# Kernel tuning notes

Hardware: AMD Instinct MI355X
Metric: run time of the kernel (lower is better)

Reference implementation:

```python
import jax, jax.numpy as jnp
import numpy as np

B, N, C = 4, 2048, 1024
H = 16
HD = C // H
SCALE = HD ** -0.5


def setup_inputs() -> dict:
    key = jax.random.key(0)
    ks = jax.random.split(key, 5)
    s = 0.02
    return {
        "x": jax.random.normal(ks[0], (B, N, C), dtype=jnp.float32),
        "w_qkv": jax.random.normal(ks[1], (C, 3 * C), dtype=jnp.float32) * s,
        "b_qkv": jnp.zeros((3 * C,), dtype=jnp.float32),
        "w_proj": jax.random.normal(ks[2], (C, C), dtype=jnp.float32) * s,
        "b_proj": jnp.zeros((C,), dtype=jnp.float32),
    }


def reference(x, w_qkv, b_qkv, w_proj, b_proj):
    b, n, c = x.shape
    qkv = x @ w_qkv + b_qkv                       # [b, n, 3c]
    qkv = qkv.reshape(b, n, 3, H, HD)
    qkv = jnp.transpose(qkv, (2, 0, 3, 1, 4))     # [3, b, h, n, hd]
    q, k, v = qkv[0], qkv[1], qkv[2]
    attn = jnp.einsum("bhqd,bhkd->bhqk", q, k) * SCALE
    attn = jax.nn.softmax(attn, axis=-1)
    out = jnp.einsum("bhqk,bhkd->bhqd", attn, v)  # [b, h, n, hd]
    out = jnp.transpose(out, (0, 2, 1, 3)).reshape(b, n, c)
    return out @ w_proj + b_proj
```

## Files before the change

### kernel.cpp

```cpp
#include <hip/hip_runtime.h>
#include <cstdint>
#include <cstddef>


typedef __attribute__((ext_vector_type(8))) short short8;
typedef __attribute__((ext_vector_type(4))) float f32x4;
typedef _Float16 half4 __attribute__((ext_vector_type(4)));

#if __has_builtin(__builtin_amdgcn_exp2f)
#define EXP2F(x) __builtin_amdgcn_exp2f(x)
#else
#define EXP2F(x) __expf((x) * 0.69314718056f)
#endif

__device__ __forceinline__ short f2bf(float x) {
  unsigned u = __builtin_bit_cast(unsigned, x);
  u += 0x7fffu + ((u >> 16) & 1u);
  return (short)(u >> 16);
}

__device__ __forceinline__ unsigned pkh(float a, float b) {
  auto h = __builtin_amdgcn_cvt_pkrtz(a, b);
  return __builtin_bit_cast(unsigned, h);
}

__device__ __forceinline__ void async16(const void* g, void* l) {
  __builtin_amdgcn_global_load_lds(
      (const __attribute__((address_space(1))) unsigned*)g,
      (__attribute__((address_space(3))) unsigned*)l, 16, 0, 0);
}

__device__ __forceinline__ void barrier_raw() {
  __asm__ volatile("" ::: "memory");
  __builtin_amdgcn_s_barrier();
  __asm__ volatile("" ::: "memory");
}


__global__ __launch_bounds__(256) void convert_kernel(const float* __restrict__ in,
                                                      short* __restrict__ out) {
  int i = blockIdx.x * 256 + threadIdx.x;
  const float4* p = (const float4*)in + (size_t)i * 2;
  float4 a = p[0], b = p[1];
  short8 r;
  r[0] = f2bf(a.x); r[1] = f2bf(a.y); r[2] = f2bf(a.z); r[3] = f2bf(a.w);
  r[4] = f2bf(b.x); r[5] = f2bf(b.y); r[6] = f2bf(b.z); r[7] = f2bf(b.w);
  *((short8*)out + i) = r;
}

__global__ __launch_bounds__(256) void wtrans_kernel(const float* __restrict__ in,
                                                     short* __restrict__ out,
                                                     int K, int N) {
  __shared__ float tile[32][33];
  int n0 = blockIdx.x * 32, k0 = blockIdx.y * 32;
  int tx = threadIdx.x, ty = threadIdx.y;
  for (int r = ty; r < 32; r += 8)
    tile[r][tx] = in[(size_t)(k0 + r) * N + n0 + tx];
  __syncthreads();
  for (int r = ty; r < 32; r += 8)
    out[(size_t)(n0 + r) * K + k0 + tx] = f2bf(tile[tx][r]);
}


template <int BM, int BN, int MODE>
__global__ __launch_bounds__(256, 2) void gemm_kernel(
    const short* __restrict__ A, const short* __restrict__ Bt,
    const float* __restrict__ bias, int Nn,
    short* __restrict__ qb, short* __restrict__ kb, short* __restrict__ vtb,
    float* __restrict__ outp) {
  constexpr int K = 1024;
  constexpr int NT = K / 32;
  constexpr int MR = BM / 32, NR = BN / 32;
  constexpr int L = (BM + BN) / 64;
  __shared__ __align__(16) short Ts[3][(BM + BN) * 32];
  const int tid = threadIdx.x, wave = tid >> 6, lane = tid & 63;
  const int quad = lane >> 4, l16 = lane & 15;

  const unsigned bid = blockIdx.x + gridDim.x * blockIdx.y;
  const unsigned c = bid & 7u, j = bid >> 3;
  const unsigned MC = gridDim.y >> 3;
  const unsigned chunk = MC * 8u;
  const unsigned nc = j / chunk, rem = j - nc * chunk;
  const unsigned m_idx = c * MC + (rem >> 3);
  const unsigned n_idx = nc * 8u + (rem & 7u);
  const int m0 = (int)m_idx * BM, n0 = (int)n_idx * BN;

  const int wrow = (wave >> 1) * (BM / 2), wcol = (wave & 1) * (BN / 2);

  const int srow = tid >> 2;
  const int sch8 = (((tid & 3) ^ (srow & 3)) * 8);
  const short* Ag = A + (size_t)(m0 + srow) * K + sch8;
  const short* Bg = Bt + (size_t)(n0 + srow) * K + sch8;
  const int fq8 = ((quad ^ (l16 & 3)) * 8);

  f32x4 acc[MR][NR] = {};

  auto stage = [&](int b, int kt) {
    char* dst = (char*)Ts[b] + tid * 16;
#pragma unroll
    for (int i = 0; i < BM / 64; ++i)
      async16(Ag + (size_t)(i * 64) * K + kt * 32, dst + i * 4096);
#pragma unroll
    for (int i = 0; i < BN / 64; ++i)
      async16(Bg + (size_t)(i * 64) * K + kt * 32, dst + (BM / 64 + i) * 4096);
  };

  stage(0, 0);
  stage(1, 1);
  if constexpr (L == 6) asm volatile("s_waitcnt vmcnt(6)" ::: "memory");
  else                  asm volatile("s_waitcnt vmcnt(4)" ::: "memory");
  barrier_raw();

  int cb = 0, sb = 2;
  for (int t = 0; t < NT; ++t) {
    if (t + 2 < NT) stage(sb, t + 2);

    const short* Tb = Ts[cb];
    short8 af[MR], bf[NR];
#pragma unroll
    for (int mf = 0; mf < MR; ++mf)
      af[mf] = *(const short8*)&Tb[(wrow + mf * 16 + l16) * 32 + fq8];
#pragma unroll
    for (int nf = 0; nf < NR; ++nf)
      bf[nf] = *(const short8*)&Tb[(BM + wcol + nf * 16 + l16) * 32 + fq8];

    __builtin_amdgcn_s_setprio(1);
#pragma unroll
    for (int mf = 0; mf < MR; ++mf)
#pragma unroll
      for (int nf = 0; nf < NR; ++nf)
        acc[mf][nf] = __builtin_amdgcn_mfma_f32_16x16x32_bf16(
            af[mf], bf[nf], acc[mf][nf], 0, 0, 0);
    __builtin_amdgcn_s_setprio(0);

    if (t + 2 < NT) {
      if constexpr (L == 6) asm volatile("s_waitcnt vmcnt(6)" ::: "memory");
      else                  asm volatile("s_waitcnt vmcnt(4)" ::: "memory");
    } else {
      asm volatile("s_waitcnt vmcnt(0)" ::: "memory");
    }
    barrier_raw();
    cb = cb + 1; if (cb >= 3) cb -= 3;
    sb = sb + 1; if (sb >= 3) sb -= 3;
  }

  if (MODE == 0) {
#pragma unroll
    for (int mf = 0; mf < MR; ++mf) {
      int row0 = m0 + wrow + mf * 16 + quad * 4;
      int b = row0 >> 11, n = row0 & 2047;
#pragma unroll
      for (int nf = 0; nf < NR; ++nf) {
        int col = n0 + wcol + nf * 16 + l16;
        float bv = bias[col];
        float v0 = acc[mf][nf][0] + bv, v1 = acc[mf][nf][1] + bv;
        float v2 = acc[mf][nf][2] + bv, v3 = acc[mf][nf][3] + bv;
        int which = col >> 10;
        int h = (col >> 6) & 15;
        int d = col & 63;
        size_t bh = (size_t)(b * 16 + h);
        if (which == 0) {
          const float qs = 0.18033688f;
          size_t base = (bh * 2048 + n) * 64 + d;
          qb[base]       = f2bf(v0 * qs);
          qb[base + 64]  = f2bf(v1 * qs);
          qb[base + 128] = f2bf(v2 * qs);
          qb[base + 192] = f2bf(v3 * qs);
        } else if (which == 1) {
          size_t base = (bh * 2048 + n) * 64 + d;
          kb[base]       = f2bf(v0);
          kb[base + 64]  = f2bf(v1);
          kb[base + 128] = f2bf(v2);
          kb[base + 192] = f2bf(v3);
        } else {
          uint2 pk;
          pk.x = pkh(v0, v1);
          pk.y = pkh(v2, v3);
          *(uint2*)&vtb[(bh * 64 + d) * 2048 + n] = pk;
        }
      }
    }
  } else {
#pragma unroll
    for (int mf = 0; mf < MR; ++mf) {
      int row0 = m0 + wrow + mf * 16 + quad * 4;
#pragma unroll
      for (int nf = 0; nf < NR; ++nf) {
        int col = n0 + wcol + nf * 16 + l16;
        float bv = bias[col];
        outp[(size_t)row0 * Nn + col]       = acc[mf][nf][0] + bv;
        outp[(size_t)(row0 + 1) * Nn + col] = acc[mf][nf][1] + bv;
        outp[(size_t)(row0 + 2) * Nn + col] = acc[mf][nf][2] + bv;
        outp[(size_t)(row0 + 3) * Nn + col] = acc[mf][nf][3] + bv;
      }
    }
  }
}


__global__ __launch_bounds__(256, 4) void attn_kernel(
    const short* __restrict__ qb, const short* __restrict__ kb,
    const short* __restrict__ vtb, short* __restrict__ ob) {
  __shared__ __align__(16) short Ks[2][64 * 64];
  __shared__ __align__(16) short Vs[2][64 * 64];
  __shared__ __align__(16) float Ls[4][32];
  const int tid = threadIdx.x, wave = tid >> 6, lane = tid & 63;
  const int quad = lane >> 4, l16 = lane & 15;
  int nlin = blockIdx.x + blockIdx.y * 16;
  nlin = (nlin & 7) * 128 + (nlin >> 3);
  const int q0 = (nlin & 15) * 128;
  const int bh = nlin >> 4;
  const short* Qg = qb + (size_t)bh * (2048 * 64);
  const short* Kg = kb + (size_t)bh * (2048 * 64);
  const short* Vg = vtb + (size_t)bh * (64 * 2048);

  short8 qf[2][2];
#pragma unroll
  for (int qt = 0; qt < 2; ++qt)
#pragma unroll
    for (int kc = 0; kc < 2; ++kc)
      qf[qt][kc] = *(const short8*)
          &Qg[(size_t)(q0 + wave * 32 + qt * 16 + l16) * 64 + kc * 32 + quad * 8];

  const int str = lane >> 3;
  const int sgc = ((lane & 7) ^ (str & 7)) * 8;
  const int fsw = l16 & 7;
  const int c0 = wave * 2, c1 = wave * 2 + 1;

  async16(Kg + (size_t)(c0 * 8 + str) * 64 + sgc, (char*)Ks[0] + c0 * 1024);
  async16(Kg + (size_t)(c1 * 8 + str) * 64 + sgc, (char*)Ks[0] + c1 * 1024);
  async16(Vg + (size_t)(c0 * 8 + str) * 2048 + sgc, (char*)Vs[0] + c0 * 1024);
  async16(Vg + (size_t)(c1 * 8 + str) * 2048 + sgc, (char*)Vs[0] + c1 * 1024);

  float lsum[2] = {0.f, 0.f};
  f32x4 oacc[2][4] = {};

  for (int t = 0; t < 32; ++t) {
    __syncthreads();

    int kvn = (t + 1) * 64;
    if (kvn < 2048) {
      char* kd = (char*)Ks[(t + 1) & 1];
      char* vd = (char*)Vs[(t + 1) & 1];
      async16(Kg + (size_t)(kvn + c0 * 8 + str) * 64 + sgc, kd + c0 * 1024);
      async16(Kg + (size_t)(kvn + c1 * 8 + str) * 64 + sgc, kd + c1 * 1024);
      async16(Vg + (size_t)(c0 * 8 + str) * 2048 + kvn + sgc, vd + c0 * 1024);
      async16(Vg + (size_t)(c1 * 8 + str) * 2048 + kvn + sgc, vd + c1 * 1024);
    }
    const short* Kst = Ks[t & 1];
    const short* Vst = Vs[t & 1];

    f32x4 sacc[2][4] = {};
#pragma unroll
    for (int kc = 0; kc < 2; ++kc) {
      short8 kf[4];
#pragma unroll
      for (int kvt = 0; kvt < 4; ++kvt)
        kf[kvt] = *(const short8*)
            &Kst[(kvt * 16 + l16) * 64 + (((kc * 4 + quad) ^ fsw) << 3)];
#pragma unroll
      for (int kvt = 0; kvt < 4; ++kvt)
#pragma unroll
        for (int qt = 0; qt < 2; ++qt)
          sacc[qt][kvt] = __builtin_amdgcn_mfma_f32_16x16x32_bf16(
              kf[kvt], qf[qt][kc], sacc[qt][kvt], 0, 0, 0);
    }

#pragma unroll
    for (int kvt = 0; kvt < 4; ++kvt) {
      half4 pfr[2];
#pragma unroll
      for (int qt = 0; qt < 2; ++qt) {
        float p0 = EXP2F(sacc[qt][kvt][0]);
        float p1 = EXP2F(sacc[qt][kvt][1]);
        float p2 = EXP2F(sacc[qt][kvt][2]);
        float p3 = EXP2F(sacc[qt][kvt][3]);
        lsum[qt] += (p0 + p1) + (p2 + p3);
        uint2 w;
        w.x = pkh(p0, p1);
        w.y = pkh(p2, p3);
        pfr[qt] = __builtin_bit_cast(half4, w);
      }
      const int vcol = (((kvt * 2 + (quad >> 1)) ^ fsw) << 3) + (quad & 1) * 4;
#pragma unroll
      for (int nt = 0; nt < 4; ++nt) {
        uint2 vr = *(const uint2*)&Vst[(nt * 16 + l16) * 64 + vcol];
        half4 vfr = __builtin_bit_cast(half4, vr);
#pragma unroll
        for (int qt = 0; qt < 2; ++qt)
          oacc[qt][nt] = __builtin_amdgcn_mfma_f32_16x16x16f16(
              pfr[qt], vfr, oacc[qt][nt], 0, 0, 0);
      }
    }
  }

#pragma unroll
  for (int qt = 0; qt < 2; ++qt) {
    float v = lsum[qt];
    v += __shfl_xor(v, 16, 64);
    v += __shfl_xor(v, 32, 64);
    if (quad == 0) Ls[wave][qt * 16 + l16] = v;
  }
  __asm__ volatile("s_waitcnt lgkmcnt(0)" ::: "memory");
  __builtin_amdgcn_wave_barrier();

  const int b = bh >> 4, h = bh & 15;
#pragma unroll
  for (int qt = 0; qt < 2; ++qt) {
    float4 lr = *(const float4*)&Ls[wave][qt * 16 + quad * 4];
    float inv0 = 1.f / lr.x, inv1 = 1.f / lr.y, inv2 = 1.f / lr.z, inv3 = 1.f / lr.w;
#pragma unroll
    for (int nt = 0; nt < 4; ++nt) {
      int d = nt * 16 + l16;
      int qbase = q0 + wave * 32 + qt * 16 + quad * 4;
      size_t obase = ((size_t)(b * 2048 + qbase)) * 1024 + h * 64 + d;
      ob[obase]        = f2bf(oacc[qt][nt][0] * inv0);
      ob[obase + 1024] = f2bf(oacc[qt][nt][1] * inv1);
      ob[obase + 2048] = f2bf(oacc[qt][nt][2] * inv2);
      ob[obase + 3072] = f2bf(oacc[qt][nt][3] * inv3);
    }
  }
}


extern "C" void kernel_launch(void* const* d_in, const int* in_sizes, int n_in,
                              void* d_out, int out_size, void* d_ws, size_t ws_size,
                              hipStream_t stream) {
  const float* x      = (const float*)d_in[0];
  const float* w_qkv  = (const float*)d_in[1];
  const float* b_qkv  = (const float*)d_in[2];
  const float* w_proj = (const float*)d_in[3];
  const float* b_proj = (const float*)d_in[4];
  float* out = (float*)d_out;

  short* xs     = (short*)d_ws;
  short* wqkvT  = xs + (size_t)8192 * 1024;
  short* wprojT = wqkvT + (size_t)3072 * 1024;
  short* qb     = wprojT + (size_t)1024 * 1024;
  short* kb     = qb + (size_t)64 * 2048 * 64;
  short* vtb    = kb + (size_t)64 * 2048 * 64;
  short* aob    = vtb + (size_t)64 * 2048 * 64;

  convert_kernel<<<dim3(4096), 256, 0, stream>>>(x, xs);
  wtrans_kernel<<<dim3(96, 32), dim3(32, 8), 0, stream>>>(w_qkv, wqkvT, 1024, 3072);
  wtrans_kernel<<<dim3(32, 32), dim3(32, 8), 0, stream>>>(w_proj, wprojT, 1024, 1024);

  gemm_kernel<256, 128, 0><<<dim3(24, 32), 256, 0, stream>>>(
      xs, wqkvT, b_qkv, 3072, qb, kb, vtb, nullptr);
  attn_kernel<<<dim3(16, 64), 256, 0, stream>>>(qb, kb, vtb, aob);
  gemm_kernel<128, 128, 1><<<dim3(8, 64), 256, 0, stream>>>(
      aob, wprojT, b_proj, 1024, nullptr, nullptr, nullptr, out);
}
```

Baseline: 276.7 us.

## Fuse prep kernels and compute softmax row sums via MFMA with ones

Merges the input conversion and the two weight-transpose kernels into one launch, which removes two kernel launch gaps. In attention, the per-row probability sums are now accumulated with an extra MFMA against a vector of ones, replacing the scalar adds, the cross-lane shuffles and the LDS round trip at the end. V fragment loads are hoisted ahead of the exp computation, and the first QK MFMA starts from a zero accumulator instead of an explicit clear. This adds MFMA work per tile in exchange for fewer VALU operations. Row sums are now formed from fp16-rounded probabilities, which changes numerics slightly.

Result: faster. 267.1 us (-3.5%).

```diff
diff --git a/kernel.cpp b/kernel.cpp
--- a/kernel.cpp
+++ b/kernel.cpp
@@ -37,23 +37,35 @@
 }
 
 
-__global__ __launch_bounds__(256) void convert_kernel(const float* __restrict__ in,
-                                                      short* __restrict__ out) {
-  int i = blockIdx.x * 256 + threadIdx.x;
-  const float4* p = (const float4*)in + (size_t)i * 2;
-  float4 a = p[0], b = p[1];
-  short8 r;
-  r[0] = f2bf(a.x); r[1] = f2bf(a.y); r[2] = f2bf(a.z); r[3] = f2bf(a.w);
-  r[4] = f2bf(b.x); r[5] = f2bf(b.y); r[6] = f2bf(b.z); r[7] = f2bf(b.w);
-  *((short8*)out + i) = r;
-}
-
-__global__ __launch_bounds__(256) void wtrans_kernel(const float* __restrict__ in,
-                                                     short* __restrict__ out,
-                                                     int K, int N) {
+__global__ __launch_bounds__(256) void prep_kernel(
+    const float* __restrict__ x, const float* __restrict__ w_qkv,
+    const float* __restrict__ w_proj, short* __restrict__ xs,
+    short* __restrict__ wqkvT, short* __restrict__ wprojT) {
   __shared__ float tile[32][33];
-  int n0 = blockIdx.x * 32, k0 = blockIdx.y * 32;
-  int tx = threadIdx.x, ty = threadIdx.y;
+  const int bid = blockIdx.x, tid = threadIdx.x;
+  if (bid < 4096) {
+    int i = bid * 256 + tid;
+    const float4* p = (const float4*)x + (size_t)i * 2;
+    float4 a = p[0], b = p[1];
+    short8 r;
+    r[0] = f2bf(a.x); r[1] = f2bf(a.y); r[2] = f2bf(a.z); r[3] = f2bf(a.w);
+    r[4] = f2bf(b.x); r[5] = f2bf(b.y); r[6] = f2bf(b.z); r[7] = f2bf(b.w);
+    *((short8*)xs + i) = r;
+    return;
+  }
+  const float* in;
+  short* out;
+  int N, bx, by;
+  if (bid < 4096 + 3072) {
+    int b = bid - 4096;
+    in = w_qkv; out = wqkvT; N = 3072; bx = b % 96; by = b / 96;
+  } else {
+    int b = bid - 7168;
+    in = w_proj; out = wprojT; N = 1024; bx = b & 31; by = b >> 5;
+  }
+  const int K = 1024;
+  int n0 = bx * 32, k0 = by * 32;
+  int tx = tid & 31, ty = tid >> 5;
   for (int r = ty; r < 32; r += 8)
     tile[r][tx] = in[(size_t)(k0 + r) * N + n0 + tx];
   __syncthreads();
@@ -203,7 +215,6 @@
     const short* __restrict__ vtb, short* __restrict__ ob) {
   __shared__ __align__(16) short Ks[2][64 * 64];
   __shared__ __align__(16) short Vs[2][64 * 64];
-  __shared__ __align__(16) float Ls[4][32];
   const int tid = threadIdx.x, wave = tid >> 6, lane = tid & 63;
   const int quad = lane >> 4, l16 = lane & 15;
   int nlin = blockIdx.x + blockIdx.y * 16;
@@ -232,8 +243,10 @@
   async16(Vg + (size_t)(c0 * 8 + str) * 2048 + sgc, (char*)Vs[0] + c0 * 1024);
   async16(Vg + (size_t)(c1 * 8 + str) * 2048 + sgc, (char*)Vs[0] + c1 * 1024);
 
-  float lsum[2] = {0.f, 0.f};
+  const half4 vone = {(_Float16)1.f, (_Float16)1.f, (_Float16)1.f, (_Float16)1.f};
+  const f32x4 fz = {};
   f32x4 oacc[2][4] = {};
+  f32x4 lacc[2] = {};
 
   for (int t = 0; t < 32; ++t) {
     __syncthreads();
@@ -250,7 +263,7 @@
     const short* Kst = Ks[t & 1];
     const short* Vst = Vs[t & 1];
 
-    f32x4 sacc[2][4] = {};
+    f32x4 sacc[2][4];
 #pragma unroll
     for (int kc = 0; kc < 2; ++kc) {
       short8 kf[4];
@@ -263,11 +276,17 @@
 #pragma unroll
         for (int qt = 0; qt < 2; ++qt)
           sacc[qt][kvt] = __builtin_amdgcn_mfma_f32_16x16x32_bf16(
-              kf[kvt], qf[qt][kc], sacc[qt][kvt], 0, 0, 0);
+              kf[kvt], qf[qt][kc], kc == 0 ? fz : sacc[qt][kvt], 0, 0, 0);
     }
 
 #pragma unroll
     for (int kvt = 0; kvt < 4; ++kvt) {
+      const int vcol = (((kvt * 2 + (quad >> 1)) ^ fsw) << 3) + (quad & 1) * 4;
+      uint2 vr[4];
+#pragma unroll
+      for (int nt = 0; nt < 4; ++nt)
+        vr[nt] = *(const uint2*)&Vst[(nt * 16 + l16) * 64 + vcol];
+
       half4 pfr[2];
 #pragma unroll
       for (int qt = 0; qt < 2; ++qt) {
@@ -275,17 +294,18 @@
         float p1 = EXP2F(sacc[qt][kvt][1]);
         float p2 = EXP2F(sacc[qt][kvt][2]);
         float p3 = EXP2F(sacc[qt][kvt][3]);
-        lsum[qt] += (p0 + p1) + (p2 + p3);
         uint2 w;
         w.x = pkh(p0, p1);
         w.y = pkh(p2, p3);
         pfr[qt] = __builtin_bit_cast(half4, w);
       }
-      const int vcol = (((kvt * 2 + (quad >> 1)) ^ fsw) << 3) + (quad & 1) * 4;
+#pragma unroll
+      for (int qt = 0; qt < 2; ++qt)
+        lacc[qt] = __builtin_amdgcn_mfma_f32_16x16x16f16(
+            pfr[qt], vone, lacc[qt], 0, 0, 0);
 #pragma unroll
       for (int nt = 0; nt < 4; ++nt) {
-        uint2 vr = *(const uint2*)&Vst[(nt * 16 + l16) * 64 + vcol];
-        half4 vfr = __builtin_bit_cast(half4, vr);
+        half4 vfr = __builtin_bit_cast(half4, vr[nt]);
 #pragma unroll
         for (int qt = 0; qt < 2; ++qt)
           oacc[qt][nt] = __builtin_amdgcn_mfma_f32_16x16x16f16(
@@ -294,21 +314,11 @@
     }
   }
 
+  const int b = bh >> 4, h = bh & 15;
 #pragma unroll
   for (int qt = 0; qt < 2; ++qt) {
-    float v = lsum[qt];
-    v += __shfl_xor(v, 16, 64);
-    v += __shfl_xor(v, 32, 64);
-    if (quad == 0) Ls[wave][qt * 16 + l16] = v;
-  }
-  __asm__ volatile("s_waitcnt lgkmcnt(0)" ::: "memory");
-  __builtin_amdgcn_wave_barrier();
-
-  const int b = bh >> 4, h = bh & 15;
-#pragma unroll
-  for (int qt = 0; qt < 2; ++qt) {
-    float4 lr = *(const float4*)&Ls[wave][qt * 16 + quad * 4];
-    float inv0 = 1.f / lr.x, inv1 = 1.f / lr.y, inv2 = 1.f / lr.z, inv3 = 1.f / lr.w;
+    float inv0 = 1.f / lacc[qt][0], inv1 = 1.f / lacc[qt][1];
+    float inv2 = 1.f / lacc[qt][2], inv3 = 1.f / lacc[qt][3];
 #pragma unroll
     for (int nt = 0; nt < 4; ++nt) {
       int d = nt * 16 + l16;
@@ -341,9 +351,8 @@
   short* vtb    = kb + (size_t)64 * 2048 * 64;
   short* aob    = vtb + (size_t)64 * 2048 * 64;
 
-  convert_kernel<<<dim3(4096), 256, 0, stream>>>(x, xs);
-  wtrans_kernel<<<dim3(96, 32), dim3(32, 8), 0, stream>>>(w_qkv, wqkvT, 1024, 3072);
-  wtrans_kernel<<<dim3(32, 32), dim3(32, 8), 0, stream>>>(w_proj, wprojT, 1024, 1024);
+  prep_kernel<<<dim3(8192), 256, 0, stream>>>(x, w_qkv, w_proj,
+                                              xs, wqkvT, wprojT);
 
   gemm_kernel<256, 128, 0><<<dim3(24, 32), 256, 0, stream>>>(
       xs, wqkvT, b_qkv, 3072, qb, kb, vtb, nullptr);
```
